# Optimization experiments

Hardware: AMD Instinct MI355X
Metric: run time of the kernel (lower is better)

The kernel has to match this reference:

```python
import jax, jax.numpy as jnp
import numpy as np
from jax import lax

# Static config (matches init_kwargs)
D_MODEL = 1024
EXPAND = 2
D_INNER = D_MODEL * EXPAND          # 2048
HEAD_DIM = 64
N_HEADS = D_INNER // HEAD_DIM       # 32
N_GROUPS = 1
D_STATE = 128
D_CONV = 4
CONV_DIM = D_INNER + 2 * N_GROUPS * D_STATE        # 2304
D_IN_PROJ = 2 * D_INNER + 2 * N_GROUPS * D_STATE + N_HEADS  # 4384
SEQLEN = 8192
LN_EPS = 1e-5


def setup_inputs() -> dict:
    key = jax.random.key(0)
    ks = jax.random.split(key, 6)
    x = jax.random.normal(ks[0], (SEQLEN, D_MODEL), jnp.float32)
    W_in = jax.random.normal(ks[1], (D_IN_PROJ, D_MODEL), jnp.float32) / np.sqrt(D_MODEL)
    W_conv = jax.random.normal(ks[2], (CONV_DIM, 1, D_CONV), jnp.float32) / np.sqrt(D_CONV)
    b_conv = jnp.zeros((CONV_DIM,), jnp.float32)
    # dt_bias init per Mamba2: dt ~ LogUniform(dt_min, dt_max), inverse-softplus
    dt = jnp.exp(jax.random.uniform(ks[3], (N_HEADS,)) * (np.log(0.1) - np.log(0.001)) + np.log(0.001))
    dt = jnp.clip(dt, 1e-4)
    dt_bias = dt + jnp.log(-jnp.expm1(-dt))
    A_log = jnp.log(jax.random.uniform(ks[4], (N_HEADS,), minval=1.0, maxval=16.0))
    D_param = jnp.ones((N_HEADS,), jnp.float32)
    ln_w = jnp.ones((D_INNER,), jnp.float32)
    ln_b = jnp.zeros((D_INNER,), jnp.float32)
    W_out = jax.random.normal(ks[5], (D_MODEL, D_INNER), jnp.float32) / np.sqrt(D_INNER)
    return dict(x=x, W_in=W_in, W_conv=W_conv, b_conv=b_conv, dt_bias=dt_bias,
                A_log=A_log, D_param=D_param, ln_w=ln_w, ln_b=ln_b, W_out=W_out)


def reference(x, W_in, W_conv, b_conv, dt_bias, A_log, D_param, ln_w, ln_b, W_out):
    L = x.shape[0]
    zxbcdt = x @ W_in.T                                   # (L, d_in_proj)
    z = zxbcdt[:, :D_INNER]                               # gate
    xbc = zxbcdt[:, D_INNER:D_INNER + CONV_DIM]           # (L, conv_dim)
    dt = jax.nn.softplus(zxbcdt[:, D_INNER + CONV_DIM:] + dt_bias)  # (L, h)
    # depthwise causal-window conv with SAME padding over the sequence
    lhs = xbc.T[None]                                      # (1, conv_dim, L)
    conv = lax.conv_general_dilated(lhs, W_conv, (1,), 'SAME',
                                    feature_group_count=CONV_DIM,
                                    dimension_numbers=('NCH', 'OIH', 'NCH'))[0]
    xbc = jax.nn.silu((conv + b_conv[:, None]).T)          # (L, conv_dim)
    x_ssm = xbc[:, :D_INNER].reshape(L, N_HEADS, HEAD_DIM)
    B = xbc[:, D_INNER:D_INNER + N_GROUPS * D_STATE].reshape(L, N_GROUPS, D_STATE)
    C = xbc[:, D_INNER + N_GROUPS * D_STATE:].reshape(L, N_GROUPS, D_STATE)
    hpg = N_HEADS // N_GROUPS
    Bh = jnp.repeat(B, hpg, axis=1)                        # (L, h, n)
    Ch = jnp.repeat(C, hpg, axis=1)                        # (L, h, n)
    A = -jnp.exp(A_log)                                    # (h,), negative
    a = jnp.exp(dt * A)                                    # (L, h) per-token decay in (0,1)
    V = x_ssm * dt[..., None]                              # discretized input (L, h, p)
    # non-causal SSD (VSSD): global state H then readout, plus D skip
    H = jnp.einsum('lhn,lh,lhp->hnp', Bh, a, V)            # (h, n, p)
    y = jnp.einsum('lhn,hnp->lhp', Ch, H) + D_param[None, :, None] * x_ssm
    y = y.reshape(L, D_INNER)
    # LayerNorm (eqx default: weight+bias, eps=1e-5), then gate by z
    mu = jnp.mean(y, axis=-1, keepdims=True)
    var = jnp.var(y, axis=-1, keepdims=True)
    y = ((y - mu) / jnp.sqrt(var + LN_EPS)) * ln_w + ln_b
    y = y * z
    return y @ W_out.T                                     # (L, d_model)
```

## Files before the change

kernel.cpp:

```cpp
#include <hip/hip_runtime.h>
#include <hip/hip_bf16.h>
#include <math.h>

#define L_SEQ 8192
#define DM 1024
#define DI 2048
#define NH 32
#define HD 64
#define DS 128
#define CDIM 2304
#define DPROJ 4384
#define NPAD_IN 4480
#define KSPLIT 16
#define OPROWS 2176

typedef short bf16x8 __attribute__((ext_vector_type(8)));
typedef float floatx4 __attribute__((ext_vector_type(4)));
typedef unsigned short u16x4 __attribute__((ext_vector_type(4)));
typedef unsigned short u16x8 __attribute__((ext_vector_type(8)));

#define AS1(p) ((const __attribute__((address_space(1))) void*)(p))
#define AS3(p) ((__attribute__((address_space(3))) void*)(p))

__device__ __forceinline__ float bf2f(unsigned short u) {
  union { unsigned int i; float f; } c; c.i = ((unsigned int)u) << 16; return c.f;
}
__device__ __forceinline__ unsigned short f2bf(float f) {
  return __bfloat16_as_ushort(__float2bfloat16(f));
}

template <int MODE>
__global__ __launch_bounds__(256)
void gemm_bt_mfma(const unsigned short* __restrict__ A, int lda,
                  const unsigned short* __restrict__ B, int ldb,
                  void* __restrict__ Cout, int ldc,
                  int Kfull, int Nstore,
                  const unsigned short* __restrict__ xs,
                  const float* __restrict__ Dvec) {
  __shared__ __align__(16) char smem[17408];
  unsigned short* Asm = (unsigned short*)smem;
  unsigned short* Bsm = Asm + 128 * 32;
  const int t = threadIdx.x;

  int bx = blockIdx.x, by = blockIdx.y;
  if (MODE != 2) {
    int gx = gridDim.x;
    int linear = by * gx + bx;
    int xcd = linear & 7;
    int local = linear >> 3;
    by = xcd * 8 + (local & 7);
    bx = local >> 3;
  }
  const int m0 = by * 128;
  const int n0 = bx * 128;

  int kstart = 0, klen = Kfull;
  if (MODE == 2) { klen = Kfull / KSPLIT; kstart = blockIdx.z * klen; }
  const int wave = t >> 6, lane = t & 63;
  const int wm = (wave & 1) * 64;
  const int wn = (wave >> 1) * 64;
  const int fr = lane & 15;
  const int quad = lane >> 4;

  floatx4 acc[4][4];
#pragma unroll
  for (int i = 0; i < 4; ++i)
#pragma unroll
    for (int j = 0; j < 4; ++j) acc[i][j] = (floatx4){0.f, 0.f, 0.f, 0.f};

  for (int k0 = kstart; k0 < kstart + klen; k0 += 32) {
#pragma unroll
    for (int i = 0; i < 2; ++i) {
      int linear = i * 256 + t;
      int row = linear >> 2;
      int kq = (linear & 3) * 8;
      const unsigned short* ga = A + (size_t)(m0 + row) * lda + (k0 + kq);
      const unsigned short* gb = B + (size_t)(n0 + row) * ldb + (k0 + kq);
      __builtin_amdgcn_global_load_lds(AS1(ga), AS3(&Asm[linear * 8]), 16, 0, 0);
      __builtin_amdgcn_global_load_lds(AS1(gb), AS3(&Bsm[linear * 8]), 16, 0, 0);
    }
    __syncthreads();

    bf16x8 af[4], bfr[4];
#pragma unroll
    for (int i = 0; i < 4; ++i) {
      af[i]  = *(const bf16x8*)&Asm[(wm + i * 16 + fr) * 32 + quad * 8];
      bfr[i] = *(const bf16x8*)&Bsm[(wn + i * 16 + fr) * 32 + quad * 8];
    }
#pragma unroll
    for (int mi = 0; mi < 4; ++mi)
#pragma unroll
      for (int ni = 0; ni < 4; ++ni)
        acc[mi][ni] = __builtin_amdgcn_mfma_f32_16x16x32_bf16(
            af[mi], bfr[ni], acc[mi][ni], 0, 0, 0);
    __syncthreads();
  }

  const int lrbase = (wm ? 16 : 0) + quad * 4;
  if (MODE == 0 || MODE == 1) {
    unsigned short(*rp)[136] = (unsigned short(*)[136])smem;
    unsigned short* C = (unsigned short*)Cout;
#pragma unroll
    for (int mi = 0; mi < 4; ++mi) {
      __syncthreads();
#pragma unroll
      for (int ni = 0; ni < 4; ++ni)
#pragma unroll
        for (int r = 0; r < 4; ++r)
          rp[lrbase + r][wn + ni * 16 + fr] = f2bf(acc[mi][ni][r]);
      __syncthreads();
#pragma unroll
      for (int j = 0; j < 2; ++j) {
        int off = j * 2048 + t * 8;
        int lr = off >> 7, c = off & 127;
        int grow = m0 + (lr >> 4) * 64 + mi * 16 + (lr & 15);
        int gcol = n0 + c;
        u16x8 v = *(const u16x8*)&rp[lr][c];
        if (MODE == 1) {
          u16x8 xv = *(const u16x8*)&xs[(size_t)grow * ldc + gcol];
          float Dh = Dvec[gcol >> 6];
          u16x8 o;
#pragma unroll
          for (int e = 0; e < 8; ++e) o[e] = f2bf(bf2f(v[e]) + Dh * bf2f(xv[e]));
          *(u16x8*)&C[(size_t)grow * ldc + gcol] = o;
        } else {
          if (gcol < Nstore) *(u16x8*)&C[(size_t)grow * ldc + gcol] = v;
        }
      }
    }
  } else {
    float(*rpf)[136] = (float(*)[136])smem;
    float* C = (float*)Cout;
    if (MODE == 2) C += (size_t)blockIdx.z * DS * DI;
#pragma unroll
    for (int mi = 0; mi < 4; ++mi) {
      __syncthreads();
#pragma unroll
      for (int ni = 0; ni < 4; ++ni)
#pragma unroll
        for (int r = 0; r < 4; ++r)
          rpf[lrbase + r][wn + ni * 16 + fr] = acc[mi][ni][r];
      __syncthreads();
#pragma unroll
      for (int j = 0; j < 4; ++j) {
        int off = j * 1024 + t * 4;
        int lr = off >> 7, c = off & 127;
        int grow = m0 + (lr >> 4) * 64 + mi * 16 + (lr & 15);
        int gcol = n0 + c;
        float4 v = *(const float4*)&rpf[lr][c];
        *(float4*)&C[(size_t)grow * ldc + gcol] = v;
      }
    }
  }
}

__global__ __launch_bounds__(256)
void cast_bf16_kernel(const float* __restrict__ in, unsigned short* __restrict__ out) {
  size_t i4 = ((size_t)blockIdx.x * 256 + threadIdx.x) * 4;
  float4 v = *(const float4*)(in + i4);
  u16x4 o;
  o.x = f2bf(v.x); o.y = f2bf(v.y); o.z = f2bf(v.z); o.w = f2bf(v.w);
  *(u16x4*)(out + i4) = o;
}

__global__ __launch_bounds__(256)
void cast_win_pad_kernel(const float* __restrict__ in, unsigned short* __restrict__ out) {
  size_t i4 = ((size_t)blockIdx.x * 256 + threadIdx.x) * 4;
  int row = (int)(i4 >> 10);
  u16x4 o = (u16x4){0, 0, 0, 0};
  if (row < DPROJ) {
    float4 v = *(const float4*)(in + i4);
    o.x = f2bf(v.x); o.y = f2bf(v.y); o.z = f2bf(v.z); o.w = f2bf(v.w);
  }
  *(u16x4*)(out + i4) = o;
}

__global__ __launch_bounds__(256)
void dt_kernel(const unsigned short* __restrict__ zxb, const float* __restrict__ dt_bias,
               const float* __restrict__ A_log, float* __restrict__ s_out) {
  int idx = blockIdx.x * 256 + threadIdx.x;
  int l = idx >> 5, h = idx & 31;
  float v = bf2f(zxb[(size_t)l * DPROJ + (DI + CDIM) + h]) + dt_bias[h];
  float d = (v > 20.f) ? v : log1pf(expf(v));
  s_out[idx] = d * expf(-d * expf(A_log[h]));
}

__global__ __launch_bounds__(256)
void conv_silu_kernel(const unsigned short* __restrict__ zxb, const float* __restrict__ Wc,
                      const float* __restrict__ bc,
                      unsigned short* __restrict__ xs,
                      unsigned short* __restrict__ bmat,
                      unsigned short* __restrict__ cb) {
  __shared__ unsigned short zt[19][256];
  const int c0 = blockIdx.x * 256;
  const int l0 = blockIdx.y * 16;
  const int t = threadIdx.x;
#pragma unroll
  for (int i = 0; i < 5; ++i) {
    int idx = i * 256 + t;
    if (idx < 19 * 64) {
      int row = idx >> 6;
      int col = (idx & 63) * 4;
      int gl = l0 - 1 + row;
      u16x4 v = (u16x4){0, 0, 0, 0};
      if (gl >= 0 && gl < L_SEQ)
        v = *(const u16x4*)&zxb[(size_t)gl * DPROJ + DI + c0 + col];
      *(u16x4*)&zt[row][col] = v;
    }
  }
  const int c = c0 + t;
  const float4 wv = *(const float4*)&Wc[c * 4];
  const float bias = bc[c];
  __syncthreads();
#pragma unroll
  for (int i = 0; i < 16; ++i) {
    int l = l0 + i;
    float s = bias + bf2f(zt[i + 0][t]) * wv.x + bf2f(zt[i + 1][t]) * wv.y +
              bf2f(zt[i + 2][t]) * wv.z + bf2f(zt[i + 3][t]) * wv.w;
    float v = s / (1.f + expf(-s));
    unsigned short b = f2bf(v);
    if (c < DI)            xs[(size_t)l * DI + c] = b;
    else if (c < DI + DS)  bmat[(size_t)l * DS + (c - DI)] = b;
    else                   cb[(size_t)l * DS + (c - DI - DS)] = b;
  }
}

__global__ __launch_bounds__(256)
void transpose_pack_kernel(const unsigned short* __restrict__ xs,
                           const unsigned short* __restrict__ bmat,
                           const float* __restrict__ s,
                           unsigned short* __restrict__ OpT) {
  __shared__ float tile[64][65];
  const int r0 = blockIdx.x * 64;
  const int l0 = blockIdx.y * 64;
  const int t = threadIdx.x;
  const bool isB = (r0 >= DI);
#pragma unroll
  for (int i = 0; i < 4; ++i) {
    int e = i * 1024 + t * 4;
    int lo = e >> 6;
    int ro = e & 63;
    int l = l0 + lo;
    u16x4 v;
    float sl;
    if (isB) {
      v = *(const u16x4*)&bmat[(size_t)l * DS + (r0 - DI) + ro];
      sl = 1.f;
    } else {
      v = *(const u16x4*)&xs[(size_t)l * DI + r0 + ro];
      sl = s[(size_t)l * NH + (r0 >> 6)];
    }
    tile[ro + 0][lo] = bf2f(v.x) * sl;
    tile[ro + 1][lo] = bf2f(v.y) * sl;
    tile[ro + 2][lo] = bf2f(v.z) * sl;
    tile[ro + 3][lo] = bf2f(v.w) * sl;
  }
  __syncthreads();
#pragma unroll
  for (int j = 0; j < 4; ++j) {
    int linear = j * 1024 + t * 4;
    int rr = linear >> 6;
    int lc = linear & 63;
    u16x4 o;
    o.x = f2bf(tile[rr][lc + 0]);
    o.y = f2bf(tile[rr][lc + 1]);
    o.z = f2bf(tile[rr][lc + 2]);
    o.w = f2bf(tile[rr][lc + 3]);
    *(u16x4*)&OpT[(size_t)(r0 + rr) * L_SEQ + l0 + lc] = o;
  }
}

__global__ __launch_bounds__(256)
void h_reduce_t_kernel(const float* __restrict__ P, unsigned short* __restrict__ Ht) {
  __shared__ float tile[32][65];
  const int bid = blockIdx.x;
  const int pt = bid & 31, ng = bid >> 5;
  const int t = threadIdx.x;
#pragma unroll
  for (int i = 0; i < 8; ++i) {
    int nl = i * 4 + (t >> 6);
    int n = ng * 32 + nl;
    int p = pt * 64 + (t & 63);
    float acc = 0.f;
#pragma unroll
    for (int z = 0; z < KSPLIT; ++z)
      acc += P[(size_t)z * (DS * DI) + (size_t)n * DI + p];
    tile[nl][t & 63] = acc;
  }
  __syncthreads();
#pragma unroll
  for (int j = 0; j < 8; ++j) {
    int linear = j * 256 + t;
    int pl = linear >> 5, nl = linear & 31;
    Ht[(size_t)(pt * 64 + pl) * DS + ng * 32 + nl] = f2bf(tile[nl][pl]);
  }
}

__global__ __launch_bounds__(256)
void ln_mul_kernel(const unsigned short* __restrict__ ybuf, unsigned short* __restrict__ zxb,
                   const float* __restrict__ ln_w, const float* __restrict__ ln_b) {
  int l = blockIdx.x;
  int t = threadIdx.x;
  int c0 = t * 8;
  u16x8 yv = *(const u16x8*)&ybuf[(size_t)l * DI + c0];
  float vals[8];
  float s = 0.f, sq = 0.f;
#pragma unroll
  for (int i = 0; i < 8; ++i) {
    float v = bf2f(yv[i]);
    vals[i] = v;
    s += v;
    sq += v * v;
  }
#pragma unroll
  for (int off = 32; off > 0; off >>= 1) {
    s += __shfl_down(s, off, 64);
    sq += __shfl_down(sq, off, 64);
  }
  __shared__ float red[10];
  int wave = t >> 6, lane = t & 63;
  if (lane == 0) { red[wave] = s; red[4 + wave] = sq; }
  __syncthreads();
  if (t == 0) {
    float S = red[0] + red[1] + red[2] + red[3];
    float SQ = red[4] + red[5] + red[6] + red[7];
    float mu = S / (float)DI;
    red[8] = mu;
    red[9] = rsqrtf(SQ / (float)DI - mu * mu + 1e-5f);
  }
  __syncthreads();
  float mu = red[8], rstd = red[9];
  unsigned short* zrow = zxb + (size_t)l * DPROJ;
  u16x8 zv = *(const u16x8*)&zrow[c0];
  float4 w0 = *(const float4*)&ln_w[c0], w1 = *(const float4*)&ln_w[c0 + 4];
  float4 b0 = *(const float4*)&ln_b[c0], b1 = *(const float4*)&ln_b[c0 + 4];
  float w[8] = {w0.x, w0.y, w0.z, w0.w, w1.x, w1.y, w1.z, w1.w};
  float b[8] = {b0.x, b0.y, b0.z, b0.w, b1.x, b1.y, b1.z, b1.w};
  u16x8 o;
#pragma unroll
  for (int i = 0; i < 8; ++i) {
    float v = (vals[i] - mu) * rstd * w[i] + b[i];
    o[i] = f2bf(v * bf2f(zv[i]));
  }
  *(u16x8*)&zrow[DI + c0] = o;
}

extern "C" void kernel_launch(void* const* d_in, const int* in_sizes, int n_in,
                              void* d_out, int out_size, void* d_ws, size_t ws_size,
                              hipStream_t stream) {
  const float* x       = (const float*)d_in[0];
  const float* W_in    = (const float*)d_in[1];
  const float* W_conv  = (const float*)d_in[2];
  const float* b_conv  = (const float*)d_in[3];
  const float* dt_bias = (const float*)d_in[4];
  const float* A_log   = (const float*)d_in[5];
  const float* D_param = (const float*)d_in[6];
  const float* ln_w    = (const float*)d_in[7];
  const float* ln_b    = (const float*)d_in[8];
  const float* W_out   = (const float*)d_in[9];
  float* out = (float*)d_out;

  unsigned short* zxb = (unsigned short*)d_ws;
  unsigned short* xs   = zxb + (size_t)L_SEQ * DPROJ;
  unsigned short* bmat = xs + (size_t)L_SEQ * DI;
  unsigned short* cb   = bmat + (size_t)L_SEQ * DS;
  float* svec = (float*)(cb + (size_t)L_SEQ * DS);
  unsigned short* OpT = (unsigned short*)(svec + (size_t)L_SEQ * NH);
  float* Ppart = (float*)(OpT + (size_t)OPROWS * L_SEQ);
  unsigned short* Ht = (unsigned short*)(Ppart + (size_t)KSPLIT * DS * DI);
  unsigned short* wout_bf16 = Ht + (size_t)DI * DS;
  unsigned short* x_bf16   = OpT;
  unsigned short* win_bf16 = OpT + (size_t)L_SEQ * DM;
  unsigned short* ybuf     = OpT;

  cast_bf16_kernel<<<(L_SEQ * DM) / 1024, 256, 0, stream>>>(x, x_bf16);
  cast_win_pad_kernel<<<(NPAD_IN * DM) / 1024, 256, 0, stream>>>(W_in, win_bf16);
  cast_bf16_kernel<<<(DM * DI) / 1024, 256, 0, stream>>>(W_out, wout_bf16);

  gemm_bt_mfma<0><<<dim3(NPAD_IN / 128, L_SEQ / 128), 256, 0, stream>>>(
      x_bf16, DM, win_bf16, DM, zxb, DPROJ, DM, DPROJ, nullptr, nullptr);

  dt_kernel<<<(L_SEQ * NH) / 256, 256, 0, stream>>>(zxb, dt_bias, A_log, svec);

  conv_silu_kernel<<<dim3(CDIM / 256, L_SEQ / 16), 256, 0, stream>>>(
      zxb, W_conv, b_conv, xs, bmat, cb);

  transpose_pack_kernel<<<dim3(OPROWS / 64, L_SEQ / 64), 256, 0, stream>>>(
      xs, bmat, svec, OpT);

  gemm_bt_mfma<2><<<dim3(DI / 128, 1, KSPLIT), 256, 0, stream>>>(
      OpT + (size_t)DI * L_SEQ, L_SEQ, OpT, L_SEQ, Ppart, DI, L_SEQ, DI,
      nullptr, nullptr);

  h_reduce_t_kernel<<<128, 256, 0, stream>>>(Ppart, Ht);

  gemm_bt_mfma<1><<<dim3(DI / 128, L_SEQ / 128), 256, 0, stream>>>(
      cb, DS, Ht, DS, ybuf, DI, DS, DI, xs, D_param);

  ln_mul_kernel<<<L_SEQ, 256, 0, stream>>>(ybuf, zxb, ln_w, ln_b);

  gemm_bt_mfma<3><<<dim3(DM / 128, L_SEQ / 128), 256, 0, stream>>>(
      zxb + DI, DPROJ, wout_bf16, DI, out, DM, DI, DM, nullptr, nullptr);
}
```

Baseline: 375.0 us.

## Fuse conv/SiLU with transpose-pack, merge cast kernels, double K-split

Merges the conv+SiLU kernel and the transpose/scale pack kernel into one kernel that computes the activated values, writes xs and C, and writes the dt-scaled, transposed B/x operand straight from shared memory. This drops the bmat buffer and a full re-read of xs. The three fp32-to-bf16 cast launches become a single launch, and KSPLIT for the state GEMM doubles to raise parallelism. The cost is a larger partial buffer for the reduction to read, and smaller channel tiles in the conv stage.

New measurement: 365.5 us. -2.6%, faster.

```diff
diff --git a/kernel.cpp b/kernel.cpp
--- a/kernel.cpp
+++ b/kernel.cpp
@@ -11,7 +11,7 @@
 #define CDIM 2304
 #define DPROJ 4384
 #define NPAD_IN 4480
-#define KSPLIT 16
+#define KSPLIT 32
 #define OPROWS 2176
 
 typedef short bf16x8 __attribute__((ext_vector_type(8)));
@@ -155,24 +155,33 @@
 }
 
 __global__ __launch_bounds__(256)
-void cast_bf16_kernel(const float* __restrict__ in, unsigned short* __restrict__ out) {
-  size_t i4 = ((size_t)blockIdx.x * 256 + threadIdx.x) * 4;
-  float4 v = *(const float4*)(in + i4);
-  u16x4 o;
-  o.x = f2bf(v.x); o.y = f2bf(v.y); o.z = f2bf(v.z); o.w = f2bf(v.w);
-  *(u16x4*)(out + i4) = o;
-}
-
-__global__ __launch_bounds__(256)
-void cast_win_pad_kernel(const float* __restrict__ in, unsigned short* __restrict__ out) {
-  size_t i4 = ((size_t)blockIdx.x * 256 + threadIdx.x) * 4;
-  int row = (int)(i4 >> 10);
+void cast_all_kernel(const float* __restrict__ x, const float* __restrict__ W_in,
+                     const float* __restrict__ W_out,
+                     unsigned short* __restrict__ x_bf16,
+                     unsigned short* __restrict__ win_bf16,
+                     unsigned short* __restrict__ wout_bf16) {
+  int b = blockIdx.x;
+  int t = threadIdx.x;
   u16x4 o = (u16x4){0, 0, 0, 0};
-  if (row < DPROJ) {
-    float4 v = *(const float4*)(in + i4);
+  if (b < 8192) {
+    size_t i4 = ((size_t)b * 256 + t) * 4;
+    float4 v = *(const float4*)(x + i4);
     o.x = f2bf(v.x); o.y = f2bf(v.y); o.z = f2bf(v.z); o.w = f2bf(v.w);
-  }
-  *(u16x4*)(out + i4) = o;
+    *(u16x4*)(x_bf16 + i4) = o;
+  } else if (b < 12672) {
+    size_t i4 = ((size_t)(b - 8192) * 256 + t) * 4;
+    int row = (int)(i4 >> 10);
+    if (row < DPROJ) {
+      float4 v = *(const float4*)(W_in + i4);
+      o.x = f2bf(v.x); o.y = f2bf(v.y); o.z = f2bf(v.z); o.w = f2bf(v.w);
+    }
+    *(u16x4*)(win_bf16 + i4) = o;
+  } else {
+    size_t i4 = ((size_t)(b - 12672) * 256 + t) * 4;
+    float4 v = *(const float4*)(W_out + i4);
+    o.x = f2bf(v.x); o.y = f2bf(v.y); o.z = f2bf(v.z); o.w = f2bf(v.w);
+    *(u16x4*)(wout_bf16 + i4) = o;
+  }
 }
 
 __global__ __launch_bounds__(256)
@@ -186,87 +195,62 @@
 }
 
 __global__ __launch_bounds__(256)
-void conv_silu_kernel(const unsigned short* __restrict__ zxb, const float* __restrict__ Wc,
-                      const float* __restrict__ bc,
-                      unsigned short* __restrict__ xs,
-                      unsigned short* __restrict__ bmat,
-                      unsigned short* __restrict__ cb) {
-  __shared__ unsigned short zt[19][256];
-  const int c0 = blockIdx.x * 256;
-  const int l0 = blockIdx.y * 16;
-  const int t = threadIdx.x;
-#pragma unroll
-  for (int i = 0; i < 5; ++i) {
-    int idx = i * 256 + t;
-    if (idx < 19 * 64) {
-      int row = idx >> 6;
-      int col = (idx & 63) * 4;
-      int gl = l0 - 1 + row;
-      u16x4 v = (u16x4){0, 0, 0, 0};
-      if (gl >= 0 && gl < L_SEQ)
-        v = *(const u16x4*)&zxb[(size_t)gl * DPROJ + DI + c0 + col];
-      *(u16x4*)&zt[row][col] = v;
-    }
-  }
-  const int c = c0 + t;
-  const float4 wv = *(const float4*)&Wc[c * 4];
-  const float bias = bc[c];
-  __syncthreads();
-#pragma unroll
-  for (int i = 0; i < 16; ++i) {
-    int l = l0 + i;
-    float s = bias + bf2f(zt[i + 0][t]) * wv.x + bf2f(zt[i + 1][t]) * wv.y +
-              bf2f(zt[i + 2][t]) * wv.z + bf2f(zt[i + 3][t]) * wv.w;
-    float v = s / (1.f + expf(-s));
-    unsigned short b = f2bf(v);
-    if (c < DI)            xs[(size_t)l * DI + c] = b;
-    else if (c < DI + DS)  bmat[(size_t)l * DS + (c - DI)] = b;
-    else                   cb[(size_t)l * DS + (c - DI - DS)] = b;
-  }
-}
-
-__global__ __launch_bounds__(256)
-void transpose_pack_kernel(const unsigned short* __restrict__ xs,
-                           const unsigned short* __restrict__ bmat,
-                           const float* __restrict__ s,
-                           unsigned short* __restrict__ OpT) {
-  __shared__ float tile[64][65];
-  const int r0 = blockIdx.x * 64;
+void conv_fused_kernel(const unsigned short* __restrict__ zxb,
+                       const float* __restrict__ Wc,
+                       const float* __restrict__ bc,
+                       const float* __restrict__ svec,
+                       unsigned short* __restrict__ xs,
+                       unsigned short* __restrict__ cb,
+                       unsigned short* __restrict__ OpT) {
+  __shared__ unsigned short zt[67][66];
+  __shared__ unsigned short ot[64][66];
+  __shared__ float sl[64];
+  const int c0 = blockIdx.x * 64;
   const int l0 = blockIdx.y * 64;
   const int t = threadIdx.x;
-  const bool isB = (r0 >= DI);
-#pragma unroll
-  for (int i = 0; i < 4; ++i) {
-    int e = i * 1024 + t * 4;
-    int lo = e >> 6;
-    int ro = e & 63;
-    int l = l0 + lo;
-    u16x4 v;
-    float sl;
-    if (isB) {
-      v = *(const u16x4*)&bmat[(size_t)l * DS + (r0 - DI) + ro];
-      sl = 1.f;
+  for (int idx = t; idx < 67 * 16; idx += 256) {
+    int row = idx >> 4;
+    int colq = (idx & 15) * 4;
+    int gl = l0 - 1 + row;
+    u16x4 v = (u16x4){0, 0, 0, 0};
+    if (gl >= 0 && gl < L_SEQ)
+      v = *(const u16x4*)&zxb[(size_t)gl * DPROJ + DI + c0 + colq];
+    *(u16x4*)&zt[row][colq] = v;
+  }
+  const bool isX = (c0 < DI);
+  const bool isC = (c0 >= DI + DS);
+  if (isX && t < 64) sl[t] = svec[(size_t)(l0 + t) * NH + (c0 >> 6)];
+  const int c = t & 63;
+  const int gc = c0 + c;
+  const float4 wv = *(const float4*)&Wc[gc * 4];
+  const float bias = bc[gc];
+  const int lq = (t >> 6) * 16;
+  __syncthreads();
+#pragma unroll
+  for (int i = 0; i < 16; ++i) {
+    int ll = lq + i;
+    float sacc = bias + bf2f(zt[ll][c]) * wv.x + bf2f(zt[ll + 1][c]) * wv.y +
+                 bf2f(zt[ll + 2][c]) * wv.z + bf2f(zt[ll + 3][c]) * wv.w;
+    float v = sacc / (1.f + expf(-sacc));
+    int gl = l0 + ll;
+    if (isC) {
+      cb[(size_t)gl * DS + (gc - (DI + DS))] = f2bf(v);
+    } else if (isX) {
+      xs[(size_t)gl * DI + gc] = f2bf(v);
+      ot[c][ll] = f2bf(v * sl[ll]);
     } else {
-      v = *(const u16x4*)&xs[(size_t)l * DI + r0 + ro];
-      sl = s[(size_t)l * NH + (r0 >> 6)];
-    }
-    tile[ro + 0][lo] = bf2f(v.x) * sl;
-    tile[ro + 1][lo] = bf2f(v.y) * sl;
-    tile[ro + 2][lo] = bf2f(v.z) * sl;
-    tile[ro + 3][lo] = bf2f(v.w) * sl;
-  }
-  __syncthreads();
-#pragma unroll
-  for (int j = 0; j < 4; ++j) {
-    int linear = j * 1024 + t * 4;
-    int rr = linear >> 6;
-    int lc = linear & 63;
-    u16x4 o;
-    o.x = f2bf(tile[rr][lc + 0]);
-    o.y = f2bf(tile[rr][lc + 1]);
-    o.z = f2bf(tile[rr][lc + 2]);
-    o.w = f2bf(tile[rr][lc + 3]);
-    *(u16x4*)&OpT[(size_t)(r0 + rr) * L_SEQ + l0 + lc] = o;
+      ot[c][ll] = f2bf(v);
+    }
+  }
+  if (!isC) {
+    __syncthreads();
+#pragma unroll
+    for (int j = 0; j < 4; ++j) {
+      int linear = j * 1024 + t * 4;
+      int rr = linear >> 6;
+      int lc = linear & 63;
+      *(u16x4*)&OpT[(size_t)(c0 + rr) * L_SEQ + l0 + lc] = *(const u16x4*)&ot[rr][lc];
+    }
   }
 }
 
@@ -362,8 +346,7 @@
 
   unsigned short* zxb = (unsigned short*)d_ws;
   unsigned short* xs   = zxb + (size_t)L_SEQ * DPROJ;
-  unsigned short* bmat = xs + (size_t)L_SEQ * DI;
-  unsigned short* cb   = bmat + (size_t)L_SEQ * DS;
+  unsigned short* cb   = xs + (size_t)L_SEQ * DI;
   float* svec = (float*)(cb + (size_t)L_SEQ * DS);
   unsigned short* OpT = (unsigned short*)(svec + (size_t)L_SEQ * NH);
   float* Ppart = (float*)(OpT + (size_t)OPROWS * L_SEQ);
@@ -373,20 +356,16 @@
   unsigned short* win_bf16 = OpT + (size_t)L_SEQ * DM;
   unsigned short* ybuf     = OpT;
 
-  cast_bf16_kernel<<<(L_SEQ * DM) / 1024, 256, 0, stream>>>(x, x_bf16);
-  cast_win_pad_kernel<<<(NPAD_IN * DM) / 1024, 256, 0, stream>>>(W_in, win_bf16);
-  cast_bf16_kernel<<<(DM * DI) / 1024, 256, 0, stream>>>(W_out, wout_bf16);
+  cast_all_kernel<<<14720, 256, 0, stream>>>(x, W_in, W_out, x_bf16, win_bf16,
+                                             wout_bf16);
 
   gemm_bt_mfma<0><<<dim3(NPAD_IN / 128, L_SEQ / 128), 256, 0, stream>>>(
       x_bf16, DM, win_bf16, DM, zxb, DPROJ, DM, DPROJ, nullptr, nullptr);
 
   dt_kernel<<<(L_SEQ * NH) / 256, 256, 0, stream>>>(zxb, dt_bias, A_log, svec);
 
-  conv_silu_kernel<<<dim3(CDIM / 256, L_SEQ / 16), 256, 0, stream>>>(
-      zxb, W_conv, b_conv, xs, bmat, cb);
-
-  transpose_pack_kernel<<<dim3(OPROWS / 64, L_SEQ / 64), 256, 0, stream>>>(
-      xs, bmat, svec, OpT);
+  conv_fused_kernel<<<dim3(CDIM / 64, L_SEQ / 64), 256, 0, stream>>>(
+      zxb, W_conv, b_conv, svec, xs, cb, OpT);
 
   gemm_bt_mfma<2><<<dim3(DI / 128, 1, KSPLIT), 256, 0, stream>>>(
       OpT + (size_t)DI * L_SEQ, L_SEQ, OpT, L_SEQ, Ppart, DI, L_SEQ, DI,
```
